# Performance work log

Hardware: AMD Instinct MI355X
Metric: run time of the kernel (lower is better)

## Reference

```python
import jax, jax.numpy as jnp
import numpy as np

B, N, D_MODEL, H, D_FF, NB_FEAT = 2, 2048, 512, 8, 2048, 256
DH = D_MODEL // H


def layer_norm(x, g, b, eps=1e-5):
    mu = jnp.mean(x, axis=-1, keepdims=True)
    var = jnp.mean((x - mu) ** 2, axis=-1, keepdims=True)
    return g * (x - mu) / jnp.sqrt(var + eps) + b


def softmax_kernel(data, proj, is_query, eps=1e-4):
    # Performer FAVOR+ positive random features. data: [b,h,n,dh], proj: [m,dh]
    dn = data.shape[-1] ** -0.25
    ratio = proj.shape[0] ** -0.5
    dd = jnp.einsum('bhnd,jd->bhnj', dn * data, proj)
    diag = (jnp.sum(data ** 2, axis=-1, keepdims=True) * 0.5) * (dn ** 2)
    if is_query:
        m = jnp.max(dd, axis=-1, keepdims=True)
    else:
        m = jnp.max(dd)
    return ratio * (jnp.exp(dd - diag - m) + eps)


def setup_inputs() -> dict:
    key = jax.random.key(0)
    ks = jax.random.split(key, 12)
    sd = D_MODEL ** -0.5
    sf = D_FF ** -0.5
    return {
        'x': jax.random.normal(ks[0], (B, N, D_MODEL), jnp.float32),
        'Wq': jax.random.normal(ks[1], (D_MODEL, D_MODEL), jnp.float32) * sd,
        'bq': jnp.zeros((D_MODEL,), jnp.float32),
        'Wk': jax.random.normal(ks[2], (D_MODEL, D_MODEL), jnp.float32) * sd,
        'bk': jnp.zeros((D_MODEL,), jnp.float32),
        'Wv': jax.random.normal(ks[3], (D_MODEL, D_MODEL), jnp.float32) * sd,
        'bv': jnp.zeros((D_MODEL,), jnp.float32),
        'Wo': jax.random.normal(ks[4], (D_MODEL, D_MODEL), jnp.float32) * sd,
        'bo': jnp.zeros((D_MODEL,), jnp.float32),
        'proj': jax.random.normal(ks[5], (NB_FEAT, DH), jnp.float32),
        'W1': jax.random.normal(ks[6], (D_MODEL, D_FF), jnp.float32) * sd,
        'b1': jnp.zeros((D_FF,), jnp.float32),
        'W2': jax.random.normal(ks[7], (D_FF, D_MODEL), jnp.float32) * sf,
        'b2': jnp.zeros((D_MODEL,), jnp.float32),
        'g1': jnp.ones((D_MODEL,), jnp.float32),
        'beta1': jnp.zeros((D_MODEL,), jnp.float32),
        'g2': jnp.ones((D_MODEL,), jnp.float32),
        'beta2': jnp.zeros((D_MODEL,), jnp.float32),
    }


def reference(x, Wq, bq, Wk, bk, Wv, bv, Wo, bo, proj, W1, b1, W2, b2, g1, beta1, g2, beta2):
    b, n, d = x.shape
    heads = lambda W, bias: (x @ W + bias).reshape(b, n, H, DH).transpose(0, 2, 1, 3)  # bhnd
    q = softmax_kernel(heads(Wq, bq), proj, is_query=True)   # [b,h,n,m]
    k = softmax_kernel(heads(Wk, bk), proj, is_query=False)  # [b,h,n,m]
    v = heads(Wv, bv)                                        # [b,h,n,dh]
    # non-causal linear attention
    k_sum = jnp.sum(k, axis=-2)                                   # [b,h,m]
    D_inv = 1.0 / jnp.einsum('bhnf,bhf->bhn', q, k_sum)           # [b,h,n]
    context = jnp.einsum('bhnf,bhne->bhfe', k, v)                 # [b,h,m,dh]
    out = jnp.einsum('bhfe,bhnf,bhn->bhne', context, q, D_inv)    # [b,h,n,dh]
    # output_attentions=True: effective attention matrix (abs, head-mean, detached)
    attn = jnp.einsum('bhnf,bhmf->bhnm', q, k) * D_inv[..., None]
    attn_weight = jax.lax.stop_gradient(jnp.mean(jnp.abs(attn), axis=1))  # [b,n,n]
    out = out.transpose(0, 2, 1, 3).reshape(b, n, d)
    out = out @ Wo + bo
    # NOTE: original module has no residual connections
    h1 = layer_norm(out, g1, beta1)
    ff = jax.nn.relu(h1 @ W1 + b1) @ W2 + b2
    y = layer_norm(ff, g2, beta2)
    return y, attn_weight
```

## Files before the change

### kernel.cpp

```cpp
#include <hip/hip_runtime.h>
#include <math.h>

#define B_SZ   2
#define N_TOK  2048
#define DM     512
#define NH     8
#define DHH    64
#define NF     256
#define DFF    2048
#define HF     2048
#define LDQKV  1536

constexpr float DN_SCALE   = 0.35355339059327373f;
constexpr float DIAG_SCALE = 0.0625f;
constexpr float RATIO      = 0.0625f;
constexpr float FEPS       = 1e-4f;
constexpr float LN_EPS     = 1e-5f;

typedef __attribute__((ext_vector_type(8))) short bf16x8;
typedef __attribute__((ext_vector_type(8))) _Float16 f16x8;
typedef __attribute__((ext_vector_type(4))) float f32x4;

__device__ __forceinline__ short f2b(float f) {
  union { float f; unsigned u; } x; x.f = f;
  unsigned r = (x.u + 0x7fff + ((x.u >> 16) & 1)) >> 16;
  return (short)r;
}
__device__ __forceinline__ float b2f(short s) {
  union { unsigned u; float f; } x; x.u = ((unsigned)(unsigned short)s) << 16;
  return x.f;
}
__device__ __forceinline__ void gload16(const void* g, void* l) {
  __builtin_amdgcn_global_load_lds((const __attribute__((address_space(1))) void*)g,
                                   (__attribute__((address_space(3))) void*)l, 16, 0, 0);
}
__device__ __forceinline__ int swz64(int row, int kbyte) {
  return (row * 128 + kbyte) ^ ((row & 7) << 4);
}
__device__ __forceinline__ float reduce_bmax512(const float* __restrict__ bmax,
                                                float* __restrict__ red) {
  int t = threadIdx.x;
  float m = fmaxf(bmax[t], bmax[t + 256]);
  #pragma unroll
  for (int o = 1; o < 64; o <<= 1) m = fmaxf(m, __shfl_xor(m, o, 64));
  if ((t & 63) == 0) red[t >> 6] = m;
  __syncthreads();
  float r = fmaxf(fmaxf(red[0], red[1]), fmaxf(red[2], red[3]));
  __syncthreads();
  return r;
}

constexpr size_t OFF_CTXP  = 0;
constexpr size_t OFF_QB    = 4194304;
constexpr size_t OFF_OUT2  = 0;
constexpr size_t OFF_FF1B  = 2097152;
constexpr size_t OFF_FF2   = 6291456;
constexpr size_t OFF_QFB   = 8388608;
constexpr size_t OFF_KB    = 12582912;
constexpr size_t OFF_QKV   = 16777216;
constexpr size_t OFF_AOB   = 20971520;
constexpr size_t OFF_H1B   = 22020096;
constexpr size_t OFF_WOT   = 23068672;
constexpr size_t OFF_W1T   = 23199744;
constexpr size_t OFF_W2T   = 23724032;
constexpr size_t OFF_KSUM  = 24248320;
constexpr size_t OFF_DINV  = 24252416;
constexpr size_t OFF_CTXT  = 24285184;
constexpr size_t OFF_BMAX  = 24416256;
constexpr size_t OFF_ROWC  = 24416832;
constexpr size_t OFF_PART  = 24420928;
constexpr size_t OFF_VSUMP = 24552000;

template<bool RELU, bool OUT_BF16, int BMODE>
__global__ __launch_bounds__(256)
void gemm_mfma(const short* __restrict__ A, const short* __restrict__ Bt,
               const float* __restrict__ bias, void* __restrict__ Cout,
               int M, int N, int K, int ldC) {
  __shared__ short As[128 * 64];
  __shared__ short Bs[128 * 64];
  int tid = threadIdx.x;
  int lane = tid & 63, wave = tid >> 6;
  int wm = wave >> 1, wn = wave & 1;
  int bm = blockIdx.y * 128, bn = blockIdx.x * 128;

  f32x4 acc[4][4] = {};
  int srow = tid >> 3;
  int scol = (tid & 7) * 8;

  for (int k0 = 0; k0 < K; k0 += 64) {
    #pragma unroll
    for (int c = 0; c < 4; ++c) {
      int r = c * 32 + srow;
      gload16(A + (size_t)(bm + r) * K + k0 + scol, As + c * 2048 + wave * 512);
      gload16(Bt + (size_t)(bn + r) * K + k0 + scol, Bs + c * 2048 + wave * 512);
    }
    __syncthreads();
    #pragma unroll
    for (int kk = 0; kk < 2; ++kk) {
      bf16x8 af[4], bf[4];
      int kq = kk * 32 + (lane >> 4) * 8;
      #pragma unroll
      for (int i = 0; i < 4; ++i)
        af[i] = *(const bf16x8*)&As[(wm * 64 + i * 16 + (lane & 15)) * 64 + kq];
      #pragma unroll
      for (int j = 0; j < 4; ++j)
        bf[j] = *(const bf16x8*)&Bs[(wn * 64 + j * 16 + (lane & 15)) * 64 + kq];
      #pragma unroll
      for (int i = 0; i < 4; ++i)
        #pragma unroll
        for (int j = 0; j < 4; ++j)
          acc[i][j] = __builtin_amdgcn_mfma_f32_16x16x32_bf16(af[i], bf[j], acc[i][j], 0, 0, 0);
    }
    __syncthreads();
  }

  int row0 = bm + wm * 64, col0 = bn + wn * 64;
  #pragma unroll
  for (int i = 0; i < 4; ++i) {
    #pragma unroll
    for (int j = 0; j < 4; ++j) {
      int col = col0 + j * 16 + (lane & 15);
      float bv = (BMODE == 1) ? bias[col] : 0.f;
      #pragma unroll
      for (int r = 0; r < 4; ++r) {
        int row = row0 + i * 16 + (lane >> 4) * 4 + r;
        float v = acc[i][j][r] + bv;
        if (RELU) v = fmaxf(v, 0.f);
        size_t off = (size_t)row * ldC + col;
        if (OUT_BF16) ((short*)Cout)[off] = f2b(v);
        else          ((float*)Cout)[off] = v;
      }
    }
  }
}

template<bool RELU, bool OUT_BF16>
__global__ __launch_bounds__(256)
void gemm_bn64(const short* __restrict__ A, const short* __restrict__ Bt,
               const float* __restrict__ bias, void* __restrict__ Cout,
               int M, int N, int K) {
  __shared__ short As[128 * 64];
  __shared__ short Bs[64 * 64];
  int tid = threadIdx.x, lane = tid & 63, wave = tid >> 6;
  int bn = blockIdx.x * 64, bm = blockIdx.y * 128;
  int srow = tid >> 3, scol = (tid & 7) * 8;
  f32x4 acc[2][4] = {};
  for (int k0 = 0; k0 < K; k0 += 64) {
    #pragma unroll
    for (int c = 0; c < 4; ++c)
      gload16(A + (size_t)(bm + c * 32 + srow) * K + k0 + scol, As + c * 2048 + wave * 512);
    #pragma unroll
    for (int c = 0; c < 2; ++c)
      gload16(Bt + (size_t)(bn + c * 32 + srow) * K + k0 + scol, Bs + c * 2048 + wave * 512);
    __syncthreads();
    #pragma unroll
    for (int kk = 0; kk < 2; ++kk) {
      bf16x8 af[2], bf[4];
      int kq = kk * 32 + (lane >> 4) * 8;
      #pragma unroll
      for (int i = 0; i < 2; ++i)
        af[i] = *(const bf16x8*)&As[(wave * 32 + i * 16 + (lane & 15)) * 64 + kq];
      #pragma unroll
      for (int j = 0; j < 4; ++j)
        bf[j] = *(const bf16x8*)&Bs[(j * 16 + (lane & 15)) * 64 + kq];
      #pragma unroll
      for (int i = 0; i < 2; ++i)
        #pragma unroll
        for (int j = 0; j < 4; ++j)
          acc[i][j] = __builtin_amdgcn_mfma_f32_16x16x32_bf16(af[i], bf[j], acc[i][j], 0, 0, 0);
    }
    __syncthreads();
  }
  #pragma unroll
  for (int i = 0; i < 2; ++i) {
    #pragma unroll
    for (int j = 0; j < 4; ++j) {
      int col = bn + j * 16 + (lane & 15);
      float bv = bias[col];
      #pragma unroll
      for (int r = 0; r < 4; ++r) {
        int row = bm + wave * 32 + i * 16 + (lane >> 4) * 4 + r;
        float v = acc[i][j][r] + bv;
        if (RELU) v = fmaxf(v, 0.f);
        if (OUT_BF16) ((short*)Cout)[(size_t)row * N + col] = f2b(v);
        else          ((float*)Cout)[(size_t)row * N + col] = v;
      }
    }
  }
}

__global__ void prep_kernel(const float* __restrict__ x, short* __restrict__ xb,
                            const float* Wq, const float* Wk, const float* Wv, const float* Wo,
                            short* Wqt, short* Wkt, short* Wvt, short* Wot,
                            const float* W1, short* W1t, const float* W2, short* W2t) {
  __shared__ float t[64][65];
  int id = blockIdx.x, tid = threadIdx.x;
  if (id >= 768) {
    size_t base = ((size_t)(id - 768) * 256 + tid) * 8;
    #pragma unroll
    for (int u = 0; u < 8; ++u) xb[base + u] = f2b(x[base + u]);
    return;
  }
  const float* W; short* Wt; int K, N, bx, by;
  if (id < 256) {
    int z = id >> 6, sub = id & 63;
    W  = (z == 0) ? Wq : (z == 1) ? Wk : (z == 2) ? Wv : Wo;
    Wt = (z == 0) ? Wqt : (z == 1) ? Wkt : (z == 2) ? Wvt : Wot;
    K = 512; N = 512; bx = sub & 7; by = sub >> 3;
  } else if (id < 512) {
    int sub = id - 256;
    W = W1; Wt = W1t; K = 512; N = 2048; bx = sub & 31; by = sub >> 5;
  } else {
    int sub = id - 512;
    W = W2; Wt = W2t; K = 2048; N = 512; bx = sub & 7; by = sub >> 3;
  }
  int k0 = by * 64, n0 = bx * 64;
  int lx = tid & 63, ly = tid >> 6;
  for (int r = ly; r < 64; r += 4)
    t[r][lx] = W[(size_t)(k0 + r) * N + n0 + lx];
  __syncthreads();
  for (int r = ly; r < 64; r += 4)
    Wt[(size_t)(n0 + r) * K + k0 + lx] = f2b(t[lx][r]);
}

__global__ __launch_bounds__(256)
void feat_mfma_kernel(const float* __restrict__ qkv, const float* __restrict__ bq,
                      const float* __restrict__ bk, const float* __restrict__ proj,
                      short* __restrict__ qfb, short* __restrict__ kbo,
                      float* __restrict__ part, float* __restrict__ bmax) {
  __shared__ short qh[64 * 64], ql[64 * 64];
  __shared__ short ph[128 * 64], pl[128 * 64];
  __shared__ float dpart[64][4];
  __shared__ float diag[64];
  __shared__ float wred[4];
  __shared__ float colp[4][256];
  int t = threadIdx.x;
  bool isq = (blockIdx.z == 0);
  int coff = isq ? 0 : 512;
  const float* bias = isq ? bq : bk;
  short* qout = isq ? qfb : kbo;
  int bh = blockIdx.y, b = bh >> 3, h = bh & 7;
  int n0 = blockIdx.x * 64;
  int lane = t & 63, w = t >> 6, l15 = lane & 15, lq = lane >> 4;

  {
    int r = t >> 2, cg = (t & 3) * 16;
    const float* src = qkv + (size_t)(b * N_TOK + n0 + r) * LDQKV + coff + h * 64 + cg;
    const float* bs = bias + h * 64 + cg;
    float ss = 0.f;
    #pragma unroll
    for (int c2 = 0; c2 < 2; ++c2) {
      f16x8 H, L;
      #pragma unroll
      for (int u = 0; u < 8; ++u) {
        float xv = src[c2 * 8 + u] + bs[c2 * 8 + u];
        ss += xv * xv;
        _Float16 hi = (_Float16)xv;
        H[u] = hi;
        L[u] = (_Float16)(xv - (float)hi);
      }
      int off = swz64(r, cg * 2 + c2 * 16);
      *(f16x8*)((char*)qh + off) = H;
      *(f16x8*)((char*)ql + off) = L;
    }
    dpart[r][t & 3] = ss;
  }
  __syncthreads();
  if (t < 64)
    diag[t] = (dpart[t][0] + dpart[t][1] + dpart[t][2] + dpart[t][3]) * DIAG_SCALE;

  f16x8 ah[2], al[2];
  #pragma unroll
  for (int kk = 0; kk < 2; ++kk) {
    int off = swz64(w * 16 + l15, kk * 64 + lq * 16);
    ah[kk] = *(f16x8*)((char*)qh + off);
    al[kk] = *(f16x8*)((char*)ql + off);
  }

  f32x4 acc[16] = {};
  #pragma unroll
  for (int half = 0; half < 2; ++half) {
    __syncthreads();
    {
      int r = t & 127, cg = (t >> 7) * 32;
      const float* src = proj + (size_t)(half * 128 + r) * DHH + cg;
      #pragma unroll
      for (int c2 = 0; c2 < 4; ++c2) {
        f16x8 H, L;
        #pragma unroll
        for (int u = 0; u < 8; ++u) {
          float xv = src[c2 * 8 + u];
          _Float16 hi = (_Float16)xv;
          H[u] = hi;
          L[u] = (_Float16)(xv - (float)hi);
        }
        int off = swz64(r, cg * 2 + c2 * 16);
        *(f16x8*)((char*)ph + off) = H;
        *(f16x8*)((char*)pl + off) = L;
      }
    }
    __syncthreads();
    #pragma unroll
    for (int jl = 0; jl < 8; ++jl) {
      int row = jl * 16 + l15;
      #pragma unroll
      for (int kk = 0; kk < 2; ++kk) {
        int off = swz64(row, kk * 64 + lq * 16);
        f16x8 bh8 = *(f16x8*)((char*)ph + off);
        f16x8 bl8 = *(f16x8*)((char*)pl + off);
        acc[half * 8 + jl] = __builtin_amdgcn_mfma_f32_16x16x32_f16(ah[kk], bh8, acc[half * 8 + jl], 0, 0, 0);
        acc[half * 8 + jl] = __builtin_amdgcn_mfma_f32_16x16x32_f16(al[kk], bh8, acc[half * 8 + jl], 0, 0, 0);
        acc[half * 8 + jl] = __builtin_amdgcn_mfma_f32_16x16x32_f16(ah[kk], bl8, acc[half * 8 + jl], 0, 0, 0);
      }
    }
  }

  if (isq) {
    #pragma unroll
    for (int r = 0; r < 4; ++r) {
      float mx = -3.4e38f;
      #pragma unroll
      for (int j = 0; j < 16; ++j) mx = fmaxf(mx, acc[j][r]);
      #pragma unroll
      for (int o = 1; o < 16; o <<= 1) mx = fmaxf(mx, __shfl_xor(mx, o, 64));
      int lrow = w * 16 + lq * 4 + r;
      float dg = diag[lrow];
      float ddm = mx * DN_SCALE;
      size_t base = (size_t)(b * N_TOK + n0 + lrow) * HF + h * NF + l15;
      #pragma unroll
      for (int j = 0; j < 16; ++j) {
        float v = RATIO * (expf(acc[j][r] * DN_SCALE - dg - ddm) + FEPS);
        qout[base + j * 16] = f2b(v);
      }
    }
  } else {
    float mxall = -3.4e38f;
    float cs[16];
    #pragma unroll
    for (int j = 0; j < 16; ++j) cs[j] = 0.f;
    #pragma unroll
    for (int r = 0; r < 4; ++r) {
      int lrow = w * 16 + lq * 4 + r;
      float dg = diag[lrow];
      size_t base = (size_t)(b * N_TOK + n0 + lrow) * HF + h * NF + l15;
      #pragma unroll
      for (int j = 0; j < 16; ++j) {
        float a = acc[j][r];
        mxall = fmaxf(mxall, a);
        float e = expf(a * DN_SCALE - dg);
        cs[j] += e;
        qout[base + j * 16] = f2b(e);
      }
    }
    #pragma unroll
    for (int j = 0; j < 16; ++j) {
      cs[j] += __shfl_xor(cs[j], 16, 64);
      cs[j] += __shfl_xor(cs[j], 32, 64);
    }
    if (lq == 0) {
      #pragma unroll
      for (int j = 0; j < 16; ++j) colp[w][j * 16 + l15] = cs[j];
    }
    #pragma unroll
    for (int o = 1; o < 64; o <<= 1) mxall = fmaxf(mxall, __shfl_xor(mxall, o, 64));
    if (lane == 0) wred[w] = mxall;
    __syncthreads();
    part[(size_t)(bh * 32 + blockIdx.x) * 256 + t] =
        colp[0][t] + colp[1][t] + colp[2][t] + colp[3][t];
    if (t == 0)
      bmax[bh * 32 + blockIdx.x] =
          fmaxf(fmaxf(wred[0], wred[1]), fmaxf(wred[2], wred[3])) * DN_SCALE;
  }
}

__global__ __launch_bounds__(256)
void ctx_part_kernel(const short* __restrict__ kb, const float* __restrict__ qkv,
                     const float* __restrict__ bv, float* __restrict__ ctxp,
                     float* __restrict__ vsump) {
  int bh = blockIdx.y, b = bh >> 3, h = bh & 7;
  int f0 = blockIdx.x * 64;
  int ns = blockIdx.z * 256;
  __shared__ float kf[32][68];
  __shared__ float vs[32][68];
  int tid = threadIdx.x;
  int tf = (tid >> 4) * 4, te = (tid & 15) * 4;
  float acc[4][4] = {};
  float vloc[4] = {};
  for (int n0 = ns; n0 < ns + 256; n0 += 32) {
    #pragma unroll
    for (int i = 0; i < 8; i++) {
      int idx = tid + i * 256;
      int nn = idx >> 6, f = idx & 63;
      kf[nn][f] = b2f(kb[(size_t)(b * N_TOK + n0 + nn) * HF + h * NF + f0 + f]);
    }
    #pragma unroll
    for (int i = 0; i < 8; i++) {
      int idx = tid + i * 256;
      int nn = idx >> 6, e = idx & 63;
      vs[nn][e] = qkv[(size_t)(b * N_TOK + n0 + nn) * LDQKV + 1024 + h * DHH + e] + bv[h * DHH + e];
    }
    __syncthreads();
    #pragma unroll
    for (int nn = 0; nn < 32; nn++) {
      float a[4], bb[4];
      #pragma unroll
      for (int i = 0; i < 4; i++) a[i] = kf[nn][tf + i];
      #pragma unroll
      for (int j = 0; j < 4; j++) bb[j] = vs[nn][te + j];
      #pragma unroll
      for (int i = 0; i < 4; i++)
        #pragma unroll
        for (int j = 0; j < 4; j++) acc[i][j] += a[i] * bb[j];
    }
    if (blockIdx.x == 0 && (tid >> 4) == 0) {
      #pragma unroll
      for (int j = 0; j < 4; j++) {
        float s = 0.f;
        for (int nn = 0; nn < 32; nn++) s += vs[nn][te + j];
        vloc[j] += s;
      }
    }
    __syncthreads();
  }
  #pragma unroll
  for (int i = 0; i < 4; i++)
    #pragma unroll
    for (int j = 0; j < 4; j++)
      ctxp[(size_t)blockIdx.z * 262144 + (size_t)bh * 16384 +
           (size_t)(f0 + tf + i) * 64 + te + j] = acc[i][j];
  if (blockIdx.x == 0 && (tid >> 4) == 0) {
    #pragma unroll
    for (int j = 0; j < 4; j++)
      vsump[((size_t)blockIdx.z * 16 + bh) * 64 + te + j] = vloc[j];
  }
}

__global__ __launch_bounds__(256)
void smallfat_kernel(const float* __restrict__ part, const float* __restrict__ bmax,
                     float* __restrict__ ksum, const float* __restrict__ ctxp,
                     const float* __restrict__ vsump, short* __restrict__ ctxT) {
  __shared__ float T[64][65];
  __shared__ float red[4];
  int t = threadIdx.x;
  float m = reduce_bmax512(bmax, red);
  float s = expf(-m);
  if (blockIdx.x < 16) {
    int bh = blockIdx.x;
    float sum = 0.f;
    #pragma unroll 8
    for (int c = 0; c < 32; ++c) sum += part[(size_t)(bh * 32 + c) * 256 + t];
    ksum[bh * 256 + t] = RATIO * (s * sum + (float)N_TOK * FEPS);
  } else {
    int id = blockIdx.x - 16;
    int ftile = id & 3, bh = id >> 2;
    int e = t & 63, q = t >> 6;
    float vsum_e = 0.f;
    #pragma unroll
    for (int c = 0; c < 8; ++c) vsum_e += vsump[((size_t)c * 16 + bh) * 64 + e];
    #pragma unroll
    for (int i = 0; i < 16; ++i) {
      int fl = i * 4 + q;
      size_t idx = (size_t)bh * 16384 + (size_t)(ftile * 64 + fl) * 64 + e;
      float sum = 0.f;
      #pragma unroll
      for (int c = 0; c < 8; ++c) sum += ctxp[(size_t)c * 262144 + idx];
      T[fl][e] = RATIO * (s * sum + FEPS * vsum_e);
    }
    __syncthreads();
    #pragma unroll
    for (int i = 0; i < 16; ++i) {
      int er = i * 4 + q;
      ctxT[(size_t)bh * 16384 + (size_t)er * 256 + ftile * 64 + e] = f2b(T[e][er]);
    }
  }
}

__global__ __launch_bounds__(256)
void dinvqs_kernel(const short* __restrict__ qfb, const float* __restrict__ ksum,
                   const float* __restrict__ bmax, float* __restrict__ Dinv,
                   float* __restrict__ rowc, short* __restrict__ qb) {
  __shared__ float red[4];
  __shared__ float wsum[4];
  int R = blockIdx.x;
  int b = R >> 11, n = R & 2047;
  int t = threadIdx.x;
  float m = reduce_bmax512(bmax, red);
  float sc = RATIO * expf(-m);
  bf16x8 qv = *(const bf16x8*)(qfb + (size_t)R * HF + t * 8);
  const float* ks = ksum + b * 2048 + t * 8;
  float p = 0.f;
  #pragma unroll
  for (int u = 0; u < 8; ++u) p += b2f(qv[u]) * ks[u];
  #pragma unroll
  for (int o = 1; o < 32; o <<= 1) p += __shfl_xor(p, o, 64);
  float d = 1.0f / p;
  if ((t & 31) == 0) Dinv[(b * NH + (t >> 5)) * N_TOK + n] = d;
  float dv = d * 0.125f;
  float qs = 0.f;
  bf16x8 o8;
  #pragma unroll
  for (int u = 0; u < 8; ++u) {
    float qb_f = b2f(qv[u]) * dv;
    qs += qb_f;
    o8[u] = f2b(qb_f * sc);
  }
  *(bf16x8*)(qb + (size_t)R * HF + t * 8) = o8;
  #pragma unroll
  for (int o = 1; o < 64; o <<= 1) qs += __shfl_xor(qs, o, 64);
  if ((t & 63) == 0) wsum[t >> 6] = qs;
  __syncthreads();
  if (t == 0) rowc[R] = RATIO * FEPS * (wsum[0] + wsum[1] + wsum[2] + wsum[3]);
}

__global__ __launch_bounds__(256)
void fat_attnw_pv(const short* __restrict__ qb, const short* __restrict__ kb,
                  const float* __restrict__ rowc, float* __restrict__ attnw,
                  const short* __restrict__ qfb, const short* __restrict__ ctxT,
                  const float* __restrict__ Dinv, short* __restrict__ aob) {
  __shared__ short As[128 * 64];
  __shared__ short Bs[128 * 64];
  int bid = blockIdx.x;
  int tid = threadIdx.x;
  int lane = tid & 63, wave = tid >> 6;
  int srow = tid >> 3, scol = (tid & 7) * 8;

  if (bid < 512) {
    int z = bid >> 8;
    int flat = bid & 255;
    int tile = flat >> 4, wi = flat & 15;
    int by = (tile >> 2) * 4 + (wi >> 2);
    int bx = (tile & 3) * 4 + (wi & 3);
    int bm = by * 128, bn = bx * 128;
    const short* Ab = qb + (size_t)z * N_TOK * HF;
    const short* Bb = kb + (size_t)z * N_TOK * HF;
    const float* rc = rowc + (size_t)z * N_TOK;
    float* out = attnw + (size_t)z * N_TOK * N_TOK;
    int wm = wave >> 1, wn = wave & 1;

    f32x4 acc[4][4] = {};
    for (int k0 = 0; k0 < HF; k0 += 64) {
      #pragma unroll
      for (int c = 0; c < 4; ++c) {
        int r = c * 32 + srow;
        gload16(Ab + (size_t)(bm + r) * HF + k0 + scol, As + c * 2048 + wave * 512);
        gload16(Bb + (size_t)(bn + r) * HF + k0 + scol, Bs + c * 2048 + wave * 512);
      }
      __syncthreads();
      #pragma unroll
      for (int kk = 0; kk < 2; ++kk) {
        bf16x8 af[4], bf[4];
        int kq = kk * 32 + (lane >> 4) * 8;
        #pragma unroll
        for (int i = 0; i < 4; ++i)
          af[i] = *(const bf16x8*)&As[(wm * 64 + i * 16 + (lane & 15)) * 64 + kq];
        #pragma unroll
        for (int j = 0; j < 4; ++j)
          bf[j] = *(const bf16x8*)&Bs[(wn * 64 + j * 16 + (lane & 15)) * 64 + kq];
        #pragma unroll
        for (int i = 0; i < 4; ++i)
          #pragma unroll
          for (int j = 0; j < 4; ++j)
            acc[i][j] = __builtin_amdgcn_mfma_f32_16x16x32_bf16(af[i], bf[j], acc[i][j], 0, 0, 0);
      }
      __syncthreads();
    }
    int row0 = bm + wm * 64, col0 = bn + wn * 64;
    #pragma unroll
    for (int i = 0; i < 4; ++i) {
      #pragma unroll
      for (int j = 0; j < 4; ++j) {
        int col = col0 + j * 16 + (lane & 15);
        #pragma unroll
        for (int r = 0; r < 4; ++r) {
          int row = row0 + i * 16 + (lane >> 4) * 4 + r;
          out[(size_t)row * N_TOK + col] = acc[i][j][r] + rc[row];
        }
      }
    }
  } else {
    int pid = bid - 512;
    int bx = pid & 15, bh = pid >> 4;
    int b = bh >> 3, h = bh & 7;
    int n0 = bx * 128;

    f32x4 acc[2][4] = {};
    for (int k0 = 0; k0 < NF; k0 += 64) {
      #pragma unroll
      for (int c = 0; c < 4; ++c) {
        int r = c * 32 + srow;
        gload16(qfb + (size_t)(b * N_TOK + n0 + r) * HF + h * NF + k0 + scol,
                As + c * 2048 + wave * 512);
      }
      #pragma unroll
      for (int c = 0; c < 2; ++c) {
        int r = c * 32 + srow;
        gload16(ctxT + (size_t)bh * 16384 + (size_t)r * 256 + k0 + scol,
                Bs + c * 2048 + wave * 512);
      }
      __syncthreads();
      #pragma unroll
      for (int kk = 0; kk < 2; ++kk) {
        bf16x8 af[2], bf[4];
        int kq = kk * 32 + (lane >> 4) * 8;
        #pragma unroll
        for (int i = 0; i < 2; ++i)
          af[i] = *(const bf16x8*)&As[(wave * 32 + i * 16 + (lane & 15)) * 64 + kq];
        #pragma unroll
        for (int j = 0; j < 4; ++j)
          bf[j] = *(const bf16x8*)&Bs[(j * 16 + (lane & 15)) * 64 + kq];
        #pragma unroll
        for (int i = 0; i < 2; ++i)
          #pragma unroll
          for (int j = 0; j < 4; ++j)
            acc[i][j] = __builtin_amdgcn_mfma_f32_16x16x32_bf16(af[i], bf[j], acc[i][j], 0, 0, 0);
      }
      __syncthreads();
    }
    #pragma unroll
    for (int i = 0; i < 2; ++i) {
      #pragma unroll
      for (int j = 0; j < 4; ++j) {
        int e = j * 16 + (lane & 15);
        #pragma unroll
        for (int r = 0; r < 4; ++r) {
          int n = n0 + wave * 32 + i * 16 + (lane >> 4) * 4 + r;
          float dv = Dinv[bh * N_TOK + n];
          aob[(size_t)(b * N_TOK + n) * DM + h * DHH + e] = f2b(acc[i][j][r] * dv);
        }
      }
    }
  }
}

template<bool OUT_BF16>
__global__ void ln_kernel(const float* __restrict__ x, const float* __restrict__ g,
                          const float* __restrict__ beta, void* __restrict__ y) {
  int row = blockIdx.x, t = threadIdx.x;
  __shared__ float red[4];
  __shared__ float bcast[2];
  const float* xr = x + (size_t)row * DM;
  float v0 = xr[t], v1 = xr[t + 256];
  float s = v0 + v1;
  #pragma unroll
  for (int o = 32; o > 0; o >>= 1) s += __shfl_xor(s, o, 64);
  if ((t & 63) == 0) red[t >> 6] = s;
  __syncthreads();
  if (t == 0) bcast[0] = (red[0] + red[1] + red[2] + red[3]) * (1.0f / 512.0f);
  __syncthreads();
  float mean = bcast[0];
  float d0 = v0 - mean, d1 = v1 - mean;
  float s2 = d0 * d0 + d1 * d1;
  #pragma unroll
  for (int o = 32; o > 0; o >>= 1) s2 += __shfl_xor(s2, o, 64);
  if ((t & 63) == 0) red[t >> 6] = s2;
  __syncthreads();
  if (t == 0) bcast[1] = (red[0] + red[1] + red[2] + red[3]) * (1.0f / 512.0f);
  __syncthreads();
  float inv = rsqrtf(bcast[1] + LN_EPS);
  float o0 = g[t] * d0 * inv + beta[t];
  float o1 = g[t + 256] * d1 * inv + beta[t + 256];
  if (OUT_BF16) {
    ((short*)y)[(size_t)row * DM + t] = f2b(o0);
    ((short*)y)[(size_t)row * DM + t + 256] = f2b(o1);
  } else {
    ((float*)y)[(size_t)row * DM + t] = o0;
    ((float*)y)[(size_t)row * DM + t + 256] = o1;
  }
}

extern "C" void kernel_launch(void* const* d_in, const int* in_sizes, int n_in,
                              void* d_out, int out_size, void* d_ws, size_t ws_size,
                              hipStream_t stream) {
  const float* x     = (const float*)d_in[0];
  const float* Wq    = (const float*)d_in[1];
  const float* bq    = (const float*)d_in[2];
  const float* Wk    = (const float*)d_in[3];
  const float* bk    = (const float*)d_in[4];
  const float* Wv    = (const float*)d_in[5];
  const float* bv    = (const float*)d_in[6];
  const float* Wo    = (const float*)d_in[7];
  const float* bo    = (const float*)d_in[8];
  const float* proj  = (const float*)d_in[9];
  const float* W1    = (const float*)d_in[10];
  const float* b1    = (const float*)d_in[11];
  const float* W2    = (const float*)d_in[12];
  const float* b2    = (const float*)d_in[13];
  const float* g1    = (const float*)d_in[14];
  const float* beta1 = (const float*)d_in[15];
  const float* g2    = (const float*)d_in[16];
  const float* beta2 = (const float*)d_in[17];

  float* ws = (float*)d_ws;
  float* y_out = (float*)d_out;
  float* attnw = y_out + (size_t)B_SZ * N_TOK * DM;

  float* ctxp  = ws + OFF_CTXP;
  short* qb    = (short*)(ws + OFF_QB);
  float* out2  = ws + OFF_OUT2;
  short* ff1b  = (short*)(ws + OFF_FF1B);
  float* ff2   = ws + OFF_FF2;
  short* qfb   = (short*)(ws + OFF_QFB);
  short* xb    = (short*)(ws + OFF_QFB);
  short* kb    = (short*)(ws + OFF_KB);
  short* Wqkvt = (short*)(ws + OFF_KB);
  float* QKVlin = ws + OFF_QKV;
  short* aob   = (short*)(ws + OFF_AOB);
  short* h1b   = (short*)(ws + OFF_H1B);
  short* Wot   = (short*)(ws + OFF_WOT);
  short* W1t   = (short*)(ws + OFF_W1T);
  short* W2t   = (short*)(ws + OFF_W2T);
  float* ksum  = ws + OFF_KSUM;
  float* Dinv  = ws + OFF_DINV;
  short* ctxT  = (short*)(ws + OFF_CTXT);
  float* bmax  = ws + OFF_BMAX;
  float* rowc  = ws + OFF_ROWC;
  float* part  = ws + OFF_PART;
  float* vsump = ws + OFF_VSUMP;

  dim3 blk(256);
  int MT = B_SZ * N_TOK;

  prep_kernel<<<1792, blk, 0, stream>>>(x, xb, Wq, Wk, Wv, Wo,
                                        Wqkvt, Wqkvt + 262144, Wqkvt + 524288, Wot,
                                        W1, W1t, W2, W2t);

  gemm_mfma<false, false, 0><<<dim3(LDQKV / 128, MT / 128), blk, 0, stream>>>(
      xb, Wqkvt, nullptr, QKVlin, MT, LDQKV, DM, LDQKV);

  feat_mfma_kernel<<<dim3(N_TOK / 64, B_SZ * NH, 2), blk, 0, stream>>>(
      QKVlin, bq, bk, proj, qfb, kb, part, bmax);

  ctx_part_kernel<<<dim3(NF / 64, B_SZ * NH, 8), blk, 0, stream>>>(kb, QKVlin, bv, ctxp, vsump);

  smallfat_kernel<<<80, blk, 0, stream>>>(part, bmax, ksum, ctxp, vsump, ctxT);

  dinvqs_kernel<<<MT, blk, 0, stream>>>(qfb, ksum, bmax, Dinv, rowc, qb);

  fat_attnw_pv<<<768, blk, 0, stream>>>(qb, kb, rowc, attnw, qfb, ctxT, Dinv, aob);

  gemm_bn64<false, false><<<dim3(DM / 64, MT / 128), blk, 0, stream>>>(
      aob, Wot, bo, out2, MT, DM, DM);

  ln_kernel<true><<<MT, blk, 0, stream>>>(out2, g1, beta1, h1b);
  gemm_mfma<true, true, 1><<<dim3(DFF / 128, MT / 128), blk, 0, stream>>>(
      h1b, W1t, b1, ff1b, MT, DFF, DM, DFF);
  gemm_bn64<false, false><<<dim3(DM / 64, MT / 128), blk, 0, stream>>>(
      ff1b, W2t, b2, ff2, MT, DM, DFF);
  ln_kernel<false><<<MT, blk, 0, stream>>>(ff2, g2, beta2, y_out);
}
```

Before: 250.1 us.

## Split attention-weight GEMM across two launches to overlap Wo projection

The attention-weight GEMM for the two batches is split across two fused kernels. The first runs batch 0 attention-weight tiles alongside the PV tiles. The second runs batch 1 attention-weight tiles alongside the Wo output projection, which depends on the PV result. This removes the separate Wo GEMM launch and hides the small projection under the large attention-weight work, at the cost of an extra dependency boundary in the middle of the attention-weight work.

```diff
diff --git a/kernel.cpp b/kernel.cpp
--- a/kernel.cpp
+++ b/kernel.cpp
@@ -71,6 +71,218 @@
 constexpr size_t OFF_PART  = 24420928;
 constexpr size_t OFF_VSUMP = 24552000;
 
+
+__device__ __forceinline__ void attnw_tile(short* As, short* Bs, int flat, int z,
+                                           const short* __restrict__ qb,
+                                           const short* __restrict__ kb,
+                                           const float* __restrict__ rowc,
+                                           float* __restrict__ attnw) {
+  int tid = threadIdx.x, lane = tid & 63, wave = tid >> 6;
+  int srow = tid >> 3, scol = (tid & 7) * 8;
+  int tile = flat >> 4, wi = flat & 15;
+  int by = (tile >> 2) * 4 + (wi >> 2);
+  int bx = (tile & 3) * 4 + (wi & 3);
+  int bm = by * 128, bn = bx * 128;
+  const short* Ab = qb + (size_t)z * N_TOK * HF;
+  const short* Bb = kb + (size_t)z * N_TOK * HF;
+  const float* rc = rowc + (size_t)z * N_TOK;
+  float* out = attnw + (size_t)z * N_TOK * N_TOK;
+  int wm = wave >> 1, wn = wave & 1;
+
+  f32x4 acc[4][4] = {};
+  for (int k0 = 0; k0 < HF; k0 += 64) {
+    #pragma unroll
+    for (int c = 0; c < 4; ++c) {
+      int r = c * 32 + srow;
+      gload16(Ab + (size_t)(bm + r) * HF + k0 + scol, As + c * 2048 + wave * 512);
+      gload16(Bb + (size_t)(bn + r) * HF + k0 + scol, Bs + c * 2048 + wave * 512);
+    }
+    __syncthreads();
+    #pragma unroll
+    for (int kk = 0; kk < 2; ++kk) {
+      bf16x8 af[4], bf[4];
+      int kq = kk * 32 + (lane >> 4) * 8;
+      #pragma unroll
+      for (int i = 0; i < 4; ++i)
+        af[i] = *(const bf16x8*)&As[(wm * 64 + i * 16 + (lane & 15)) * 64 + kq];
+      #pragma unroll
+      for (int j = 0; j < 4; ++j)
+        bf[j] = *(const bf16x8*)&Bs[(wn * 64 + j * 16 + (lane & 15)) * 64 + kq];
+      #pragma unroll
+      for (int i = 0; i < 4; ++i)
+        #pragma unroll
+        for (int j = 0; j < 4; ++j)
+          acc[i][j] = __builtin_amdgcn_mfma_f32_16x16x32_bf16(af[i], bf[j], acc[i][j], 0, 0, 0);
+    }
+    __syncthreads();
+  }
+  int row0 = bm + wm * 64, col0 = bn + wn * 64;
+  #pragma unroll
+  for (int i = 0; i < 4; ++i) {
+    #pragma unroll
+    for (int j = 0; j < 4; ++j) {
+      int col = col0 + j * 16 + (lane & 15);
+      #pragma unroll
+      for (int r = 0; r < 4; ++r) {
+        int row = row0 + i * 16 + (lane >> 4) * 4 + r;
+        out[(size_t)row * N_TOK + col] = acc[i][j][r] + rc[row];
+      }
+    }
+  }
+}
+
+__device__ __forceinline__ void pv_tile(short* As, short* Bs, int pid,
+                                        const short* __restrict__ qfb,
+                                        const short* __restrict__ ctxT,
+                                        const float* __restrict__ Dinv,
+                                        short* __restrict__ aob) {
+  int tid = threadIdx.x, lane = tid & 63, wave = tid >> 6;
+  int srow = tid >> 3, scol = (tid & 7) * 8;
+  int bx = pid & 15, bh = pid >> 4;
+  int b = bh >> 3, h = bh & 7;
+  int n0 = bx * 128;
+
+  f32x4 acc[2][4] = {};
+  for (int k0 = 0; k0 < NF; k0 += 64) {
+    #pragma unroll
+    for (int c = 0; c < 4; ++c) {
+      int r = c * 32 + srow;
+      gload16(qfb + (size_t)(b * N_TOK + n0 + r) * HF + h * NF + k0 + scol,
+              As + c * 2048 + wave * 512);
+    }
+    #pragma unroll
+    for (int c = 0; c < 2; ++c) {
+      int r = c * 32 + srow;
+      gload16(ctxT + (size_t)bh * 16384 + (size_t)r * 256 + k0 + scol,
+              Bs + c * 2048 + wave * 512);
+    }
+    __syncthreads();
+    #pragma unroll
+    for (int kk = 0; kk < 2; ++kk) {
+      bf16x8 af[2], bf[4];
+      int kq = kk * 32 + (lane >> 4) * 8;
+      #pragma unroll
+      for (int i = 0; i < 2; ++i)
+        af[i] = *(const bf16x8*)&As[(wave * 32 + i * 16 + (lane & 15)) * 64 + kq];
+      #pragma unroll
+      for (int j = 0; j < 4; ++j)
+        bf[j] = *(const bf16x8*)&Bs[(j * 16 + (lane & 15)) * 64 + kq];
+      #pragma unroll
+      for (int i = 0; i < 2; ++i)
+        #pragma unroll
+        for (int j = 0; j < 4; ++j)
+          acc[i][j] = __builtin_amdgcn_mfma_f32_16x16x32_bf16(af[i], bf[j], acc[i][j], 0, 0, 0);
+    }
+    __syncthreads();
+  }
+  #pragma unroll
+  for (int i = 0; i < 2; ++i) {
+    #pragma unroll
+    for (int j = 0; j < 4; ++j) {
+      int e = j * 16 + (lane & 15);
+      #pragma unroll
+      for (int r = 0; r < 4; ++r) {
+        int n = n0 + wave * 32 + i * 16 + (lane >> 4) * 4 + r;
+        float dv = Dinv[bh * N_TOK + n];
+        aob[(size_t)(b * N_TOK + n) * DM + h * DHH + e] = f2b(acc[i][j][r] * dv);
+      }
+    }
+  }
+}
+
+template<bool RELU, bool OUT_BF16>
+__device__ __forceinline__ void bn64_tile(short* As, short* Bs, int bn, int bm,
+                                          const short* __restrict__ A,
+                                          const short* __restrict__ Bt,
+                                          const float* __restrict__ bias,
+                                          void* __restrict__ Cout, int N, int K) {
+  int tid = threadIdx.x, lane = tid & 63, wave = tid >> 6;
+  int srow = tid >> 3, scol = (tid & 7) * 8;
+  f32x4 acc[2][4] = {};
+  for (int k0 = 0; k0 < K; k0 += 64) {
+    #pragma unroll
+    for (int c = 0; c < 4; ++c)
+      gload16(A + (size_t)(bm + c * 32 + srow) * K + k0 + scol, As + c * 2048 + wave * 512);
+    #pragma unroll
+    for (int c = 0; c < 2; ++c)
+      gload16(Bt + (size_t)(bn + c * 32 + srow) * K + k0 + scol, Bs + c * 2048 + wave * 512);
+    __syncthreads();
+    #pragma unroll
+    for (int kk = 0; kk < 2; ++kk) {
+      bf16x8 af[2], bf[4];
+      int kq = kk * 32 + (lane >> 4) * 8;
+      #pragma unroll
+      for (int i = 0; i < 2; ++i)
+        af[i] = *(const bf16x8*)&As[(wave * 32 + i * 16 + (lane & 15)) * 64 + kq];
+      #pragma unroll
+      for (int j = 0; j < 4; ++j)
+        bf[j] = *(const bf16x8*)&Bs[(j * 16 + (lane & 15)) * 64 + kq];
+      #pragma unroll
+      for (int i = 0; i < 2; ++i)
+        #pragma unroll
+        for (int j = 0; j < 4; ++j)
+          acc[i][j] = __builtin_amdgcn_mfma_f32_16x16x32_bf16(af[i], bf[j], acc[i][j], 0, 0, 0);
+    }
+    __syncthreads();
+  }
+  #pragma unroll
+  for (int i = 0; i < 2; ++i) {
+    #pragma unroll
+    for (int j = 0; j < 4; ++j) {
+      int col = bn + j * 16 + (lane & 15);
+      float bv = bias[col];
+      #pragma unroll
+      for (int r = 0; r < 4; ++r) {
+        int row = bm + wave * 32 + i * 16 + (lane >> 4) * 4 + r;
+        float v = acc[i][j][r] + bv;
+        if (RELU) v = fmaxf(v, 0.f);
+        if (OUT_BF16) ((short*)Cout)[(size_t)row * N + col] = f2b(v);
+        else          ((float*)Cout)[(size_t)row * N + col] = v;
+      }
+    }
+  }
+}
+
+
+__global__ __launch_bounds__(256)
+void fat1_kernel(const short* __restrict__ qb, const short* __restrict__ kb,
+                 const float* __restrict__ rowc, float* __restrict__ attnw,
+                 const short* __restrict__ qfb, const short* __restrict__ ctxT,
+                 const float* __restrict__ Dinv, short* __restrict__ aob) {
+  __shared__ short As[128 * 64];
+  __shared__ short Bs[128 * 64];
+  int bid = blockIdx.x;
+  if (bid < 256) attnw_tile(As, Bs, bid, 0, qb, kb, rowc, attnw);
+  else           pv_tile(As, Bs, bid - 256, qfb, ctxT, Dinv, aob);
+}
+
+__global__ __launch_bounds__(256)
+void fat2_kernel(const short* __restrict__ qb, const short* __restrict__ kb,
+                 const float* __restrict__ rowc, float* __restrict__ attnw,
+                 const short* __restrict__ aob, const short* __restrict__ Wot,
+                 const float* __restrict__ bo, float* __restrict__ out2) {
+  __shared__ short As[128 * 64];
+  __shared__ short Bs[128 * 64];
+  int bid = blockIdx.x;
+  if (bid < 256) {
+    attnw_tile(As, Bs, bid, 1, qb, kb, rowc, attnw);
+  } else {
+    int pid = bid - 256;
+    bn64_tile<false, false>(As, Bs, (pid & 7) * 64, (pid >> 3) * 128,
+                            aob, Wot, bo, out2, DM, DM);
+  }
+}
+
+template<bool RELU, bool OUT_BF16>
+__global__ __launch_bounds__(256)
+void gemm_bn64(const short* __restrict__ A, const short* __restrict__ Bt,
+               const float* __restrict__ bias, void* __restrict__ Cout,
+               int M, int N, int K) {
+  __shared__ short As[128 * 64];
+  __shared__ short Bs[64 * 64];
+  bn64_tile<RELU, OUT_BF16>(As, Bs, blockIdx.x * 64, blockIdx.y * 128, A, Bt, bias, Cout, N, K);
+}
+
 template<bool RELU, bool OUT_BF16, int BMODE>
 __global__ __launch_bounds__(256)
 void gemm_mfma(const short* __restrict__ A, const short* __restrict__ Bt,
@@ -129,61 +341,6 @@
         size_t off = (size_t)row * ldC + col;
         if (OUT_BF16) ((short*)Cout)[off] = f2b(v);
         else          ((float*)Cout)[off] = v;
-      }
-    }
-  }
-}
-
-template<bool RELU, bool OUT_BF16>
-__global__ __launch_bounds__(256)
-void gemm_bn64(const short* __restrict__ A, const short* __restrict__ Bt,
-               const float* __restrict__ bias, void* __restrict__ Cout,
-               int M, int N, int K) {
-  __shared__ short As[128 * 64];
-  __shared__ short Bs[64 * 64];
-  int tid = threadIdx.x, lane = tid & 63, wave = tid >> 6;
-  int bn = blockIdx.x * 64, bm = blockIdx.y * 128;
-  int srow = tid >> 3, scol = (tid & 7) * 8;
-  f32x4 acc[2][4] = {};
-  for (int k0 = 0; k0 < K; k0 += 64) {
-    #pragma unroll
-    for (int c = 0; c < 4; ++c)
-      gload16(A + (size_t)(bm + c * 32 + srow) * K + k0 + scol, As + c * 2048 + wave * 512);
-    #pragma unroll
-    for (int c = 0; c < 2; ++c)
-      gload16(Bt + (size_t)(bn + c * 32 + srow) * K + k0 + scol, Bs + c * 2048 + wave * 512);
-    __syncthreads();
-    #pragma unroll
-    for (int kk = 0; kk < 2; ++kk) {
-      bf16x8 af[2], bf[4];
-      int kq = kk * 32 + (lane >> 4) * 8;
-      #pragma unroll
-      for (int i = 0; i < 2; ++i)
-        af[i] = *(const bf16x8*)&As[(wave * 32 + i * 16 + (lane & 15)) * 64 + kq];
-      #pragma unroll
-      for (int j = 0; j < 4; ++j)
-        bf[j] = *(const bf16x8*)&Bs[(j * 16 + (lane & 15)) * 64 + kq];
-      #pragma unroll
-      for (int i = 0; i < 2; ++i)
-        #pragma unroll
-        for (int j = 0; j < 4; ++j)
-          acc[i][j] = __builtin_amdgcn_mfma_f32_16x16x32_bf16(af[i], bf[j], acc[i][j], 0, 0, 0);
-    }
-    __syncthreads();
-  }
-  #pragma unroll
-  for (int i = 0; i < 2; ++i) {
-    #pragma unroll
-    for (int j = 0; j < 4; ++j) {
-      int col = bn + j * 16 + (lane & 15);
-      float bv = bias[col];
-      #pragma unroll
-      for (int r = 0; r < 4; ++r) {
-        int row = bm + wave * 32 + i * 16 + (lane >> 4) * 4 + r;
-        float v = acc[i][j][r] + bv;
-        if (RELU) v = fmaxf(v, 0.f);
-        if (OUT_BF16) ((short*)Cout)[(size_t)row * N + col] = f2b(v);
-        else          ((float*)Cout)[(size_t)row * N + col] = v;
       }
     }
   }
@@ -510,126 +667,6 @@
   if ((t & 63) == 0) wsum[t >> 6] = qs;
   __syncthreads();
   if (t == 0) rowc[R] = RATIO * FEPS * (wsum[0] + wsum[1] + wsum[2] + wsum[3]);
-}
-
-__global__ __launch_bounds__(256)
-void fat_attnw_pv(const short* __restrict__ qb, const short* __restrict__ kb,
-                  const float* __restrict__ rowc, float* __restrict__ attnw,
-                  const short* __restrict__ qfb, const short* __restrict__ ctxT,
-                  const float* __restrict__ Dinv, short* __restrict__ aob) {
-  __shared__ short As[128 * 64];
-  __shared__ short Bs[128 * 64];
-  int bid = blockIdx.x;
-  int tid = threadIdx.x;
-  int lane = tid & 63, wave = tid >> 6;
-  int srow = tid >> 3, scol = (tid & 7) * 8;
-
-  if (bid < 512) {
-    int z = bid >> 8;
-    int flat = bid & 255;
-    int tile = flat >> 4, wi = flat & 15;
-    int by = (tile >> 2) * 4 + (wi >> 2);
-    int bx = (tile & 3) * 4 + (wi & 3);
-    int bm = by * 128, bn = bx * 128;
-    const short* Ab = qb + (size_t)z * N_TOK * HF;
-    const short* Bb = kb + (size_t)z * N_TOK * HF;
-    const float* rc = rowc + (size_t)z * N_TOK;
-    float* out = attnw + (size_t)z * N_TOK * N_TOK;
-    int wm = wave >> 1, wn = wave & 1;
-
-    f32x4 acc[4][4] = {};
-    for (int k0 = 0; k0 < HF; k0 += 64) {
-      #pragma unroll
-      for (int c = 0; c < 4; ++c) {
-        int r = c * 32 + srow;
-        gload16(Ab + (size_t)(bm + r) * HF + k0 + scol, As + c * 2048 + wave * 512);
-        gload16(Bb + (size_t)(bn + r) * HF + k0 + scol, Bs + c * 2048 + wave * 512);
-      }
-      __syncthreads();
-      #pragma unroll
-      for (int kk = 0; kk < 2; ++kk) {
-        bf16x8 af[4], bf[4];
-        int kq = kk * 32 + (lane >> 4) * 8;
-        #pragma unroll
-        for (int i = 0; i < 4; ++i)
-          af[i] = *(const bf16x8*)&As[(wm * 64 + i * 16 + (lane & 15)) * 64 + kq];
-        #pragma unroll
-        for (int j = 0; j < 4; ++j)
-          bf[j] = *(const bf16x8*)&Bs[(wn * 64 + j * 16 + (lane & 15)) * 64 + kq];
-        #pragma unroll
-        for (int i = 0; i < 4; ++i)
-          #pragma unroll
-          for (int j = 0; j < 4; ++j)
-            acc[i][j] = __builtin_amdgcn_mfma_f32_16x16x32_bf16(af[i], bf[j], acc[i][j], 0, 0, 0);
-      }
-      __syncthreads();
-    }
-    int row0 = bm + wm * 64, col0 = bn + wn * 64;
-    #pragma unroll
-    for (int i = 0; i < 4; ++i) {
-      #pragma unroll
-      for (int j = 0; j < 4; ++j) {
-        int col = col0 + j * 16 + (lane & 15);
-        #pragma unroll
-        for (int r = 0; r < 4; ++r) {
-          int row = row0 + i * 16 + (lane >> 4) * 4 + r;
-          out[(size_t)row * N_TOK + col] = acc[i][j][r] + rc[row];
-        }
-      }
-    }
-  } else {
-    int pid = bid - 512;
-    int bx = pid & 15, bh = pid >> 4;
-    int b = bh >> 3, h = bh & 7;
-    int n0 = bx * 128;
-
-    f32x4 acc[2][4] = {};
-    for (int k0 = 0; k0 < NF; k0 += 64) {
-      #pragma unroll
-      for (int c = 0; c < 4; ++c) {
-        int r = c * 32 + srow;
-        gload16(qfb + (size_t)(b * N_TOK + n0 + r) * HF + h * NF + k0 + scol,
-                As + c * 2048 + wave * 512);
-      }
-      #pragma unroll
-      for (int c = 0; c < 2; ++c) {
-        int r = c * 32 + srow;
-        gload16(ctxT + (size_t)bh * 16384 + (size_t)r * 256 + k0 + scol,
-                Bs + c * 2048 + wave * 512);
-      }
-      __syncthreads();
-      #pragma unroll
-      for (int kk = 0; kk < 2; ++kk) {
-        bf16x8 af[2], bf[4];
-        int kq = kk * 32 + (lane >> 4) * 8;
-        #pragma unroll
-        for (int i = 0; i < 2; ++i)
-          af[i] = *(const bf16x8*)&As[(wave * 32 + i * 16 + (lane & 15)) * 64 + kq];
-        #pragma unroll
-        for (int j = 0; j < 4; ++j)
-          bf[j] = *(const bf16x8*)&Bs[(j * 16 + (lane & 15)) * 64 + kq];
-        #pragma unroll
-        for (int i = 0; i < 2; ++i)
-          #pragma unroll
-          for (int j = 0; j < 4; ++j)
-            acc[i][j] = __builtin_amdgcn_mfma_f32_16x16x32_bf16(af[i], bf[j], acc[i][j], 0, 0, 0);
-      }
-      __syncthreads();
-    }
-    #pragma unroll
-    for (int i = 0; i < 2; ++i) {
-      #pragma unroll
-      for (int j = 0; j < 4; ++j) {
-        int e = j * 16 + (lane & 15);
-        #pragma unroll
-        for (int r = 0; r < 4; ++r) {
-          int n = n0 + wave * 32 + i * 16 + (lane >> 4) * 4 + r;
-          float dv = Dinv[bh * N_TOK + n];
-          aob[(size_t)(b * N_TOK + n) * DM + h * DHH + e] = f2b(acc[i][j][r] * dv);
-        }
-      }
-    }
-  }
 }
 
 template<bool OUT_BF16>
@@ -736,10 +773,9 @@
 
   dinvqs_kernel<<<MT, blk, 0, stream>>>(qfb, ksum, bmax, Dinv, rowc, qb);
 
-  fat_attnw_pv<<<768, blk, 0, stream>>>(qb, kb, rowc, attnw, qfb, ctxT, Dinv, aob);
-
-  gemm_bn64<false, false><<<dim3(DM / 64, MT / 128), blk, 0, stream>>>(
-      aob, Wot, bo, out2, MT, DM, DM);
+  fat1_kernel<<<512, blk, 0, stream>>>(qb, kb, rowc, attnw, qfb, ctxT, Dinv, aob);
+
+  fat2_kernel<<<512, blk, 0, stream>>>(qb, kb, rowc, attnw, aob, Wot, bo, out2);
 
   ln_kernel<true><<<MT, blk, 0, stream>>>(out2, g1, beta1, h1b);
   gemm_mfma<true, true, 1><<<dim3(DFF / 128, MT / 128), blk, 0, stream>>>(
```

After: 275.2 us. +10.0%, slower.
